# Kernel optimization log

Measured on AMD Instinct MI355X. Metric: run time of the kernel, lower is better.

Reference implementation:

```python
import jax, jax.numpy as jnp
import numpy as np

N, E, K, IN, OUT = 20000, 320000, 5, 256, 128
NAN_FRAC = 0.3


def setup_inputs() -> dict:
    key = jax.random.key(0)
    ks = jax.random.split(key, 8)
    x = jax.random.normal(ks[0], (N, IN), dtype=jnp.float32)
    nan_mask = jax.random.uniform(ks[1], (N, IN)) < NAN_FRAC
    x = jnp.where(nan_mask, jnp.nan, x)  # missing features as NaN
    edge_index = jax.random.randint(ks[2], (2, E), 0, N, dtype=jnp.int64)
    logp = jax.nn.log_softmax(jax.random.normal(ks[3], (K,), dtype=jnp.float32))
    means = jax.random.normal(ks[4], (K, IN), dtype=jnp.float32)
    logvars = jax.random.normal(ks[5], (K, IN), dtype=jnp.float32) * 0.1
    xav = 1.414 * np.sqrt(6.0 / (IN + OUT))
    weight = jax.random.uniform(ks[6], (IN, OUT), dtype=jnp.float32, minval=-xav, maxval=xav)
    bias = jnp.zeros((OUT,), dtype=jnp.float32)
    return {"x": x, "edge_index": edge_index, "logp": logp, "means": means,
            "logvars": logvars, "weight": weight, "bias": bias}


def _ex_relu(mu, sigma):
    # E[relu(X)] for X ~ N(mu, sigma); sigma is the variance
    sigma_s = jnp.where(sigma == 0, 1e-10, sigma)
    ss = jnp.sqrt(sigma_s)
    w = mu / ss
    nr = ss * (jnp.exp(-0.5 * w * w) / np.sqrt(2 * np.pi)
               + 0.5 * w * (1.0 + jax.lax.erf(w / np.sqrt(2))))
    return jnp.where(sigma == 0, jnp.maximum(mu, 0.0), nr)


def _gcn_norm(edge_index, num_nodes):
    # add self-loops, symmetric D^-1/2 A D^-1/2 normalization
    row = jnp.concatenate([edge_index[0], jnp.arange(num_nodes, dtype=edge_index.dtype)])
    col = jnp.concatenate([edge_index[1], jnp.arange(num_nodes, dtype=edge_index.dtype)])
    ones = jnp.ones(row.shape[0], dtype=jnp.float32)
    deg = jax.ops.segment_sum(ones, row, num_segments=num_nodes)
    dinv = jnp.where(deg > 0, jax.lax.rsqrt(deg), 0.0)
    wn = dinv[row] * dinv[col]
    return row, col, wn


def reference(x, edge_index, logp, means, logvars, weight, bias):
    n = x.shape[0]
    dim = x.shape[1]
    row, col, wn = _gcn_norm(edge_index, n)
    wn2 = wn * wn  # adj2 = adj * adj (elementwise on sparse values)

    isnan = jnp.isnan(x)                                       # [N, IN]
    variances = jnp.exp(logvars)                               # [K, IN]
    mean_mat = jnp.where(isnan[None], means[:, None, :], x[None])      # [K, N, IN]
    var_mat = jnp.where(isnan[None], variances[:, None, :], 0.0)       # [K, N, IN]

    transform_x = jnp.einsum('kni,io->kno', mean_mat, weight) + bias   # [K, N, OUT]
    transform_covs = jnp.einsum('kni,io->kno', var_mat, weight * weight)

    def spmm(vals, X):  # segment-sum SpMM: out[r] += vals_e * X[c]
        return jax.ops.segment_sum(X[col] * vals[:, None], row, num_segments=n)

    conv_x = jax.vmap(lambda X: spmm(wn, X))(transform_x)      # [K, N, OUT]
    conv_covs = jax.vmap(lambda X: spmm(wn2, X))(transform_covs)

    expected_x = _ex_relu(conv_x, conv_covs)                   # [K, N, OUT]

    # GMM responsibilities per node
    log_n = (-0.5 * jnp.sum((mean_mat - means[:, None, :]) ** 2 / variances[:, None, :], axis=2)
             - 0.5 * dim * np.log(2 * np.pi) - 0.5 * jnp.sum(logvars))  # [K, N]
    gamma = jax.nn.softmax(logp[:, None] + log_n, axis=0)      # [K, N]

    return jnp.sum(expected_x * gamma[:, :, None], axis=0)     # [N, OUT]
```

## Files before the change

### kernel.cpp

```cpp
#include <hip/hip_runtime.h>
#include <stdint.h>

#define N_NODES 20000
#define N_EDGES 320000
#define K_MIX 5
#define IN_F 256
#define OUT_F 128
#define NT 11
#define TC (NT * OUT_F)

typedef __attribute__((ext_vector_type(8))) short short8;
typedef __attribute__((ext_vector_type(4))) float floatx4;

__device__ __forceinline__ float bf2f(unsigned int u) {
  union { unsigned int i; float f; } v;
  v.i = (u & 0xffffu) << 16;
  return v.f;
}
__device__ __forceinline__ unsigned short f2bf(float f) {
  union { float f; unsigned int i; } v;
  v.f = f;
  unsigned int x = v.i;
  unsigned int r = (x + 0x7fffu + ((x >> 16) & 1u)) >> 16;
  return (unsigned short)r;
}

__device__ __forceinline__ float exrelu(float mu, float sig) {
  if (sig < 1e-30f) return fmaxf(mu, 0.f);
  float ss = sqrtf(sig);
  float w = mu / ss;
  float e = __expf(-0.5f * w * w);
  float axv = fabsf(w) * 0.70710678118654752f;
  float t = 1.f / (1.f + 0.3275911f * axv);
  float poly = t * (0.254829592f +
              t * (-0.284496736f +
              t * (1.421413741f +
              t * (-1.453152027f + t * 1.061405429f))));
  float erfv = 1.f - poly * e;
  erfv = copysignf(erfv, w);
  return ss * (e * 0.3989422804014327f + 0.5f * w * (1.f + erfv));
}

__global__ void k_deg(const int* __restrict__ row, int* __restrict__ deg) {
  int t = blockIdx.x * 256 + threadIdx.x;
  if (t < N_EDGES) atomicAdd(&deg[row[t]], 1);
}

__global__ void k_scan1(const int* __restrict__ deg, int* __restrict__ startofs,
                        int* __restrict__ bsums, float* __restrict__ dinv) {
  __shared__ int sd[256];
  int t = threadIdx.x;
  int i = blockIdx.x * 256 + t;
  int v = (i < N_NODES) ? deg[i] : 0;
  if (i < N_NODES) dinv[i] = rsqrtf((float)(v + 1));
  sd[t] = v;
  __syncthreads();
  for (int off = 1; off < 256; off <<= 1) {
    int u = (t >= off) ? sd[t - off] : 0;
    __syncthreads();
    sd[t] += u;
    __syncthreads();
  }
  if (i < N_NODES) startofs[i] = sd[t] - v;
  if (t == 255) bsums[blockIdx.x] = sd[255];
}

__global__ void k_scan2(int* __restrict__ bsums, int nb) {
  __shared__ int sd[128];
  int t = threadIdx.x;
  int v = (t < nb) ? bsums[t] : 0;
  sd[t] = v;
  __syncthreads();
  for (int off = 1; off < 128; off <<= 1) {
    int u = (t >= off) ? sd[t - off] : 0;
    __syncthreads();
    sd[t] += u;
    __syncthreads();
  }
  if (t < nb) bsums[t] = sd[t] - v;
}

__global__ void k_scan3(int* __restrict__ startofs, int* __restrict__ cursor,
                        const int* __restrict__ bsums) {
  int i = blockIdx.x * 256 + threadIdx.x;
  if (i < N_NODES) {
    int s0 = startofs[i] + bsums[blockIdx.x];
    startofs[i] = s0;
    cursor[i] = s0;
  }
}

__global__ void k_scatter(const int* __restrict__ row, const int* __restrict__ col,
                          const float* __restrict__ dinv, int* __restrict__ cursor,
                          int* __restrict__ csr_col, float* __restrict__ csr_w) {
  int t = blockIdx.x * 256 + threadIdx.x;
  if (t < N_EDGES) {
    int r = row[t], c = col[t];
    int p = atomicAdd(&cursor[r], 1);
    csr_col[p] = c;
    csr_w[p] = dinv[r] * dinv[c];
  }
}

__global__ void k_buildB(const float* __restrict__ W, const float* __restrict__ means,
                         const float* __restrict__ logvars, unsigned short* __restrict__ Bt) {
  int idx = blockIdx.x * 256 + threadIdx.x;
  int j = idx >> 15;
  int rem = idx & 32767;
  int n = rem >> 8;
  int kk = rem & 255;
  float wv = W[kk * OUT_F + n];
  float val;
  if (j == 0) val = wv;
  else if (j <= 5) val = means[(j - 1) * IN_F + kk] * wv;
  else val = expf(logvars[(j - 6) * IN_F + kk]) * wv * wv;
  Bt[idx] = f2bf(val);
}

__global__ void k_prepx(const float* __restrict__ x, const float* __restrict__ logp,
                        const float* __restrict__ means, const float* __restrict__ logvars,
                        unsigned short* __restrict__ X0, float* __restrict__ gamma) {
  __shared__ float s_mean[K_MIX * IN_F];
  __shared__ float s_rv[K_MIX * IN_F];
  int t = threadIdx.x;
  for (int j = t; j < K_MIX * IN_F; j += 256) {
    s_mean[j] = means[j];
    s_rv[j] = expf(-logvars[j]);
  }
  __syncthreads();
  int node = blockIdx.x * 4 + (t >> 6);
  if (node >= N_NODES) return;
  int lane = t & 63;
  float4 xv = *(const float4*)(x + (size_t)node * IN_F + 4 * lane);
  float xf[4] = {xv.x, xv.y, xv.z, xv.w};
  float gsum[K_MIX] = {0, 0, 0, 0, 0};
  ushort4 o;
  unsigned short* op = (unsigned short*)&o;
#pragma unroll
  for (int j = 0; j < 4; j++) {
    bool nn = (xf[j] != xf[j]);
    op[j] = nn ? (unsigned short)0x7FC0 : f2bf(xf[j]);
    if (!nn) {
      int fi = 4 * lane + j;
#pragma unroll
      for (int k = 0; k < K_MIX; k++) {
        float d = xf[j] - s_mean[k * IN_F + fi];
        gsum[k] += d * d * s_rv[k * IN_F + fi];
      }
    }
  }
  *(ushort4*)(X0 + node * IN_F + 4 * lane) = o;
#pragma unroll
  for (int k = 0; k < K_MIX; k++)
    for (int off = 32; off; off >>= 1) gsum[k] += __shfl_xor(gsum[k], off, 64);
  if (lane == 0) {
    float lg[K_MIX], mx = -1e30f;
#pragma unroll
    for (int k = 0; k < K_MIX; k++) {
      lg[k] = logp[k] - 0.5f * gsum[k];
      mx = fmaxf(mx, lg[k]);
    }
    float se = 0.f;
#pragma unroll
    for (int k = 0; k < K_MIX; k++) { lg[k] = expf(lg[k] - mx); se += lg[k]; }
    float inv = 1.f / se;
#pragma unroll
    for (int k = 0; k < K_MIX; k++) gamma[node * K_MIX + k] = lg[k] * inv;
  }
}

__global__ __launch_bounds__(64) void k_spmm(const unsigned short* __restrict__ X0,
                       const int* __restrict__ startofs, const int* __restrict__ deg,
                       const float* __restrict__ dinv, const int* __restrict__ csr_col,
                       const float* __restrict__ csr_w, unsigned short* __restrict__ G,
                       float* __restrict__ sArr) {
  int node = blockIdx.x;
  int lane = threadIdx.x;
  int fo = 4 * lane;
  float ax[4] = {0, 0, 0, 0}, am[4] = {0, 0, 0, 0}, am2[4] = {0, 0, 0, 0};
  float ssum = 0.f;
  float ws = dinv[node];
  ws = ws * ws;
  int st = startofs[node];
  int total = deg[node] + 1;
  ushort4 zero4 = {0, 0, 0, 0};
  ushort4 B0 = zero4, B1 = zero4, B2 = zero4, B3 = zero4,
          B4 = zero4, B5 = zero4, B6 = zero4, B7 = zero4;
  float W0 = 0.f, W1 = 0.f, W2 = 0.f, W3 = 0.f,
        W4 = 0.f, W5 = 0.f, W6 = 0.f, W7 = 0.f;
  B0 = *(const ushort4*)(X0 + node * IN_F + fo); W0 = ws;
#define PFILL(S)                                                      \
  if (S < total) {                                                    \
    int c = csr_col[st + (S - 1)];                                    \
    W##S = csr_w[st + (S - 1)];                                       \
    B##S = *(const ushort4*)(X0 + c * IN_F + fo);                     \
  }
  PFILL(1) PFILL(2) PFILL(3) PFILL(4) PFILL(5) PFILL(6) PFILL(7)
#undef PFILL

#define STEP(S)                                                       \
  if (W##S != 0.f) {                                                  \
    float wv = W##S, wv2 = wv * wv;                                   \
    ssum += wv;                                                       \
    const unsigned short* xp = (const unsigned short*)&B##S;          \
    _Pragma("unroll")                                                 \
    for (int j = 0; j < 4; j++) {                                     \
      float xf = bf2f(xp[j]);                                         \
      bool nn = (xf != xf);                                           \
      ax[j] = fmaf(wv, nn ? 0.f : xf, ax[j]);                         \
      am[j] += nn ? wv : 0.f;                                         \
      am2[j] += nn ? wv2 : 0.f;                                       \
    }                                                                 \
  }                                                                   \
  if (base + 8 + S < total) {                                         \
    int c = csr_col[st + base + 7 + S];                               \
    W##S = csr_w[st + base + 7 + S];                                  \
    B##S = *(const ushort4*)(X0 + c * IN_F + fo);                     \
  } else {                                                            \
    W##S = 0.f;                                                       \
  }

  for (int base = 0; base < total; base += 8) {
    STEP(0) STEP(1) STEP(2) STEP(3) STEP(4) STEP(5) STEP(6) STEP(7)
  }
#undef STEP

  ushort4 o;
  o.x = f2bf(ax[0]); o.y = f2bf(ax[1]); o.z = f2bf(ax[2]); o.w = f2bf(ax[3]);
  *(ushort4*)(G + node * 768 + fo) = o;
  o.x = f2bf(am[0]); o.y = f2bf(am[1]); o.z = f2bf(am[2]); o.w = f2bf(am[3]);
  *(ushort4*)(G + node * 768 + 256 + fo) = o;
  o.x = f2bf(am2[0]); o.y = f2bf(am2[1]); o.z = f2bf(am2[2]); o.w = f2bf(am2[3]);
  *(ushort4*)(G + node * 768 + 512 + fo) = o;
  if (lane == 0) sArr[node] = ssum;
}

__global__ __launch_bounds__(256) void k_gemm(const unsigned short* __restrict__ G,
                                              const unsigned short* __restrict__ Bt,
                                              unsigned short* __restrict__ T) {
  __shared__ char Als[128 * 64 * 2];
  __shared__ char Bls[128 * 64 * 2];
  int mt = blockIdx.x, jt = blockIdx.y;
  int aoff = (jt == 0) ? 0 : (jt <= 5 ? 256 : 512);
  int t = threadIdx.x, wave = t >> 6, lane = t & 63;
  int wr = wave >> 1, wc = wave & 1;
  int quad = lane >> 4, l16 = lane & 15;
  const unsigned short* Bp = Bt + (size_t)jt * 32768;

  floatx4 acc[4][4];
  floatx4 z = {0.f, 0.f, 0.f, 0.f};
#pragma unroll
  for (int mi = 0; mi < 4; mi++)
#pragma unroll
    for (int ni = 0; ni < 4; ni++) acc[mi][ni] = z;

  for (int k0 = 0; k0 < 256; k0 += 64) {
    __syncthreads();
#pragma unroll
    for (int i = 0; i < 4; i++) {
      int f = i * 256 + t;
      int r = f >> 3, cchunk = f & 7;
      int sw = cchunk ^ (r & 7);
      int gr = mt * 128 + r;
      if (gr >= N_NODES) gr = N_NODES - 1;
      *(uint4*)(Als + r * 128 + sw * 16) =
          *(const uint4*)(G + (size_t)gr * 768 + aoff + k0 + cchunk * 8);
      *(uint4*)(Bls + r * 128 + sw * 16) =
          *(const uint4*)(Bp + (size_t)r * 256 + k0 + cchunk * 8);
    }
    __syncthreads();
#pragma unroll
    for (int ks = 0; ks < 2; ks++) {
      int cc = ks * 4 + quad;
      short8 a[4], b[4];
#pragma unroll
      for (int mi = 0; mi < 4; mi++) {
        int r = wr * 64 + mi * 16 + l16;
        a[mi] = *(const short8*)(Als + r * 128 + (cc ^ (r & 7)) * 16);
      }
#pragma unroll
      for (int ni = 0; ni < 4; ni++) {
        int r = wc * 64 + ni * 16 + l16;
        b[ni] = *(const short8*)(Bls + r * 128 + (cc ^ (r & 7)) * 16);
      }
#pragma unroll
      for (int mi = 0; mi < 4; mi++)
#pragma unroll
        for (int ni = 0; ni < 4; ni++)
          acc[mi][ni] = __builtin_amdgcn_mfma_f32_16x16x32_bf16(a[mi], b[ni], acc[mi][ni], 0, 0, 0);
    }
  }
#pragma unroll
  for (int mi = 0; mi < 4; mi++)
#pragma unroll
    for (int ni = 0; ni < 4; ni++) {
      int gc = jt * 128 + wc * 64 + ni * 16 + l16;
#pragma unroll
      for (int reg = 0; reg < 4; reg++) {
        int gr = mt * 128 + wr * 64 + mi * 16 + quad * 4 + reg;
        if (gr < N_NODES) T[(size_t)gr * TC + gc] = f2bf(acc[mi][ni][reg]);
      }
    }
}

__global__ void k_final(const unsigned short* __restrict__ T, const float* __restrict__ gamma,
                        const float* __restrict__ sArr, const float* __restrict__ bias,
                        float* __restrict__ out) {
  int t = threadIdx.x;
  int node = blockIdx.x * 4 + (t >> 6);
  if (node >= N_NODES) return;
  int lane = t & 63;
  int o0 = 2 * lane;
  float g[K_MIX];
#pragma unroll
  for (int k = 0; k < K_MIX; k++) g[k] = gamma[node * K_MIX + k];
  float sv = sArr[node];
  float b0 = bias[o0], b1 = bias[o0 + 1];
  const unsigned short* Tr = T + (size_t)node * TC;
  unsigned int c0u = *(const unsigned int*)(Tr + o0);
  float cx0 = bf2f(c0u), cx1 = bf2f(c0u >> 16);
  float a0 = 0.f, a1 = 0.f;
#pragma unroll
  for (int k = 0; k < K_MIX; k++) {
    unsigned int tm = *(const unsigned int*)(Tr + 128 * (1 + k) + o0);
    unsigned int tv = *(const unsigned int*)(Tr + 128 * (6 + k) + o0);
    float mu0 = cx0 + bf2f(tm) + b0 * sv;
    float mu1 = cx1 + bf2f(tm >> 16) + b1 * sv;
    a0 += g[k] * exrelu(mu0, bf2f(tv));
    a1 += g[k] * exrelu(mu1, bf2f(tv >> 16));
  }
  float2 ov = {a0, a1};
  *(float2*)(out + (size_t)node * OUT_F + o0) = ov;
}

extern "C" void kernel_launch(void* const* d_in, const int* in_sizes, int n_in,
                              void* d_out, int out_size, void* d_ws, size_t ws_size,
                              hipStream_t stream) {
  const float* x = (const float*)d_in[0];
  const int* ei = (const int*)d_in[1];
  const float* logp = (const float*)d_in[2];
  const float* means = (const float*)d_in[3];
  const float* lvar = (const float*)d_in[4];
  const float* W = (const float*)d_in[5];
  const float* bias = (const float*)d_in[6];
  float* out = (float*)d_out;
  const int* row = ei;
  const int* col = ei + N_EDGES;

  char* p = (char*)d_ws;
  auto alloc = [&](size_t bytes) -> char* {
    char* q = p;
    p += (bytes + 255) & ~((size_t)255);
    return q;
  };
  int* deg = (int*)alloc(N_NODES * 4);
  float* dinv = (float*)alloc(N_NODES * 4);
  int* startofs = (int*)alloc(N_NODES * 4);
  int* cursor = (int*)alloc(N_NODES * 4);
  int* bsums = (int*)alloc(128 * 4);
  int* csr_col = (int*)alloc((size_t)N_EDGES * 4);
  float* csr_w = (float*)alloc((size_t)N_EDGES * 4);
  float* gamma = (float*)alloc((size_t)N_NODES * K_MIX * 4);
  float* sArr = (float*)alloc(N_NODES * 4);
  unsigned short* Bt = (unsigned short*)alloc((size_t)NT * 128 * 256 * 2);
  unsigned short* X0 = (unsigned short*)alloc((size_t)N_NODES * IN_F * 2);
  unsigned short* G = (unsigned short*)alloc((size_t)N_NODES * 768 * 2);
  unsigned short* T = (unsigned short*)alloc((size_t)N_NODES * TC * 2);

  hipMemsetAsync(deg, 0, N_NODES * 4, stream);
  k_deg<<<(N_EDGES + 255) / 256, 256, 0, stream>>>(row, deg);
  k_scan1<<<79, 256, 0, stream>>>(deg, startofs, bsums, dinv);
  k_scan2<<<1, 128, 0, stream>>>(bsums, 79);
  k_scan3<<<79, 256, 0, stream>>>(startofs, cursor, bsums);
  k_scatter<<<(N_EDGES + 255) / 256, 256, 0, stream>>>(row, col, dinv, cursor, csr_col, csr_w);
  k_buildB<<<(NT * 128 * 256) / 256, 256, 0, stream>>>(W, means, lvar, Bt);
  k_prepx<<<N_NODES / 4, 256, 0, stream>>>(x, logp, means, lvar, X0, gamma);
  k_spmm<<<N_NODES, 64, 0, stream>>>(X0, startofs, deg, dinv, csr_col, csr_w, G, sArr);
  k_gemm<<<dim3((N_NODES + 127) / 128, NT), 256, 0, stream>>>(G, Bt, T);
  k_final<<<N_NODES / 4, 256, 0, stream>>>(T, gamma, sArr, bias, out);
}
```

Before: 230.1 us.

## Fuse GEMM with expected-ReLU mixture epilogue, removing intermediate T buffer

```diff
diff --git a/kernel.cpp b/kernel.cpp
--- a/kernel.cpp
+++ b/kernel.cpp
@@ -7,7 +7,6 @@
 #define IN_F 256
 #define OUT_F 128
 #define NT 11
-#define TC (NT * OUT_F)
 
 typedef __attribute__((ext_vector_type(8))) short short8;
 typedef __attribute__((ext_vector_type(4))) float floatx4;
@@ -235,102 +234,87 @@
   if (lane == 0) sArr[node] = ssum;
 }
 
-__global__ __launch_bounds__(256) void k_gemm(const unsigned short* __restrict__ G,
-                                              const unsigned short* __restrict__ Bt,
-                                              unsigned short* __restrict__ T) {
-  __shared__ char Als[128 * 64 * 2];
-  __shared__ char Bls[128 * 64 * 2];
-  int mt = blockIdx.x, jt = blockIdx.y;
-  int aoff = (jt == 0) ? 0 : (jt <= 5 ? 256 : 512);
+__global__ __launch_bounds__(256) void k_gemmE(const unsigned short* __restrict__ G,
+                                               const unsigned short* __restrict__ Bt,
+                                               const float* __restrict__ gamma,
+                                               const float* __restrict__ sArr,
+                                               const float* __restrict__ bias,
+                                               float* __restrict__ out) {
+  __shared__ char Als[3 * 4 * 128 * 16];
+  __shared__ float lgam[128 * K_MIX];
+  __shared__ float ls[128];
+  int mt = blockIdx.x, ng = blockIdx.y;
+  int row0 = mt * 128;
   int t = threadIdx.x, wave = t >> 6, lane = t & 63;
-  int wr = wave >> 1, wc = wave & 1;
   int quad = lane >> 4, l16 = lane & 15;
-  const unsigned short* Bp = Bt + (size_t)jt * 32768;
-
-  floatx4 acc[4][4];
+
+  for (int i = t; i < 128 * K_MIX; i += 256) {
+    int node = row0 + i / K_MIX;
+    lgam[i] = (node < N_NODES) ? gamma[node * K_MIX + i % K_MIX] : 0.f;
+  }
+  if (t < 128) {
+    int node = row0 + t;
+    ls[t] = (node < N_NODES) ? sArr[node] : 0.f;
+  }
+  int colg = ng * 16 + l16;
+  float bc = bias[colg];
+  const unsigned short* Bcol = Bt + colg * 256 + quad * 8;
+
+  floatx4 acc[2][NT];
   floatx4 z = {0.f, 0.f, 0.f, 0.f};
 #pragma unroll
-  for (int mi = 0; mi < 4; mi++)
-#pragma unroll
-    for (int ni = 0; ni < 4; ni++) acc[mi][ni] = z;
-
-  for (int k0 = 0; k0 < 256; k0 += 64) {
-    __syncthreads();
-#pragma unroll
-    for (int i = 0; i < 4; i++) {
+  for (int m = 0; m < 2; m++)
+#pragma unroll
+    for (int j = 0; j < NT; j++) acc[m][j] = z;
+
+  int rbase = wave * 32;
+  for (int k0 = 0; k0 < 256; k0 += 32) {
+    __syncthreads();
+#pragma unroll
+    for (int i = 0; i < 6; i++) {
       int f = i * 256 + t;
-      int r = f >> 3, cchunk = f & 7;
-      int sw = cchunk ^ (r & 7);
-      int gr = mt * 128 + r;
+      int q = f & 3;
+      int r = (f >> 2) & 127;
+      int s = f >> 9;
+      int gr = row0 + r;
       if (gr >= N_NODES) gr = N_NODES - 1;
-      *(uint4*)(Als + r * 128 + sw * 16) =
-          *(const uint4*)(G + (size_t)gr * 768 + aoff + k0 + cchunk * 8);
-      *(uint4*)(Bls + r * 128 + sw * 16) =
-          *(const uint4*)(Bp + (size_t)r * 256 + k0 + cchunk * 8);
-    }
-    __syncthreads();
-#pragma unroll
-    for (int ks = 0; ks < 2; ks++) {
-      int cc = ks * 4 + quad;
-      short8 a[4], b[4];
-#pragma unroll
-      for (int mi = 0; mi < 4; mi++) {
-        int r = wr * 64 + mi * 16 + l16;
-        a[mi] = *(const short8*)(Als + r * 128 + (cc ^ (r & 7)) * 16);
+      *(uint4*)(Als + s * 8192 + q * 2048 + ((r ^ (q * 2)) & 127) * 16) =
+          *(const uint4*)(G + gr * 768 + s * 256 + k0 + q * 8);
+    }
+    __syncthreads();
+    short8 af[3][2];
+#pragma unroll
+    for (int s = 0; s < 3; s++)
+#pragma unroll
+      for (int m = 0; m < 2; m++) {
+        int r = rbase + m * 16 + l16;
+        af[s][m] = *(const short8*)(Als + s * 8192 + quad * 2048 +
+                                    ((r ^ (quad * 2)) & 127) * 16);
       }
 #pragma unroll
-      for (int ni = 0; ni < 4; ni++) {
-        int r = wc * 64 + ni * 16 + l16;
-        b[ni] = *(const short8*)(Bls + r * 128 + (cc ^ (r & 7)) * 16);
-      }
-#pragma unroll
-      for (int mi = 0; mi < 4; mi++)
-#pragma unroll
-        for (int ni = 0; ni < 4; ni++)
-          acc[mi][ni] = __builtin_amdgcn_mfma_f32_16x16x32_bf16(a[mi], b[ni], acc[mi][ni], 0, 0, 0);
-    }
-  }
-#pragma unroll
-  for (int mi = 0; mi < 4; mi++)
-#pragma unroll
-    for (int ni = 0; ni < 4; ni++) {
-      int gc = jt * 128 + wc * 64 + ni * 16 + l16;
-#pragma unroll
-      for (int reg = 0; reg < 4; reg++) {
-        int gr = mt * 128 + wr * 64 + mi * 16 + quad * 4 + reg;
-        if (gr < N_NODES) T[(size_t)gr * TC + gc] = f2bf(acc[mi][ni][reg]);
-      }
-    }
-}
-
-__global__ void k_final(const unsigned short* __restrict__ T, const float* __restrict__ gamma,
-                        const float* __restrict__ sArr, const float* __restrict__ bias,
-                        float* __restrict__ out) {
-  int t = threadIdx.x;
-  int node = blockIdx.x * 4 + (t >> 6);
-  if (node >= N_NODES) return;
-  int lane = t & 63;
-  int o0 = 2 * lane;
-  float g[K_MIX];
-#pragma unroll
-  for (int k = 0; k < K_MIX; k++) g[k] = gamma[node * K_MIX + k];
-  float sv = sArr[node];
-  float b0 = bias[o0], b1 = bias[o0 + 1];
-  const unsigned short* Tr = T + (size_t)node * TC;
-  unsigned int c0u = *(const unsigned int*)(Tr + o0);
-  float cx0 = bf2f(c0u), cx1 = bf2f(c0u >> 16);
-  float a0 = 0.f, a1 = 0.f;
-#pragma unroll
-  for (int k = 0; k < K_MIX; k++) {
-    unsigned int tm = *(const unsigned int*)(Tr + 128 * (1 + k) + o0);
-    unsigned int tv = *(const unsigned int*)(Tr + 128 * (6 + k) + o0);
-    float mu0 = cx0 + bf2f(tm) + b0 * sv;
-    float mu1 = cx1 + bf2f(tm >> 16) + b1 * sv;
-    a0 += g[k] * exrelu(mu0, bf2f(tv));
-    a1 += g[k] * exrelu(mu1, bf2f(tv >> 16));
-  }
-  float2 ov = {a0, a1};
-  *(float2*)(out + (size_t)node * OUT_F + o0) = ov;
+    for (int j = 0; j < NT; j++) {
+      int s = (j == 0) ? 0 : (j <= 5 ? 1 : 2);
+      short8 b = *(const short8*)(Bcol + j * 32768 + k0);
+      acc[0][j] = __builtin_amdgcn_mfma_f32_16x16x32_bf16(af[s][0], b, acc[0][j], 0, 0, 0);
+      acc[1][j] = __builtin_amdgcn_mfma_f32_16x16x32_bf16(af[s][1], b, acc[1][j], 0, 0, 0);
+    }
+  }
+
+#pragma unroll
+  for (int m = 0; m < 2; m++) {
+#pragma unroll
+    for (int reg = 0; reg < 4; reg++) {
+      int rl = rbase + m * 16 + quad * 4 + reg;
+      int node = row0 + rl;
+      float sv = ls[rl];
+      float cx = acc[m][0][reg] + bc * sv;
+      float a = 0.f;
+#pragma unroll
+      for (int k = 0; k < K_MIX; k++)
+        a += lgam[rl * K_MIX + k] * exrelu(cx + acc[m][1 + k][reg], acc[m][6 + k][reg]);
+      if (node < N_NODES) out[node * OUT_F + colg] = a;
+    }
+  }
 }
 
 extern "C" void kernel_launch(void* const* d_in, const int* in_sizes, int n_in,
@@ -365,7 +349,6 @@
   unsigned short* Bt = (unsigned short*)alloc((size_t)NT * 128 * 256 * 2);
   unsigned short* X0 = (unsigned short*)alloc((size_t)N_NODES * IN_F * 2);
   unsigned short* G = (unsigned short*)alloc((size_t)N_NODES * 768 * 2);
-  unsigned short* T = (unsigned short*)alloc((size_t)N_NODES * TC * 2);
 
   hipMemsetAsync(deg, 0, N_NODES * 4, stream);
   k_deg<<<(N_EDGES + 255) / 256, 256, 0, stream>>>(row, deg);
@@ -376,6 +359,5 @@
   k_buildB<<<(NT * 128 * 256) / 256, 256, 0, stream>>>(W, means, lvar, Bt);
   k_prepx<<<N_NODES / 4, 256, 0, stream>>>(x, logp, means, lvar, X0, gamma);
   k_spmm<<<N_NODES, 64, 0, stream>>>(X0, startofs, deg, dinv, csr_col, csr_w, G, sArr);
-  k_gemm<<<dim3((N_NODES + 127) / 128, NT), 256, 0, stream>>>(G, Bt, T);
-  k_final<<<N_NODES / 4, 256, 0, stream>>>(T, gamma, sArr, bias, out);
-}
+  k_gemmE<<<dim3((N_NODES + 127) / 128, 8), 256, 0, stream>>>(G, Bt, gamma, sArr, bias, out);
+}
```

New measurement: 283.7 us. +23.3%, slower.

## Precompute NaN mask in prep layout, hoist exp(-logvar), XCD-aware GEMM tile mapping

Applied to the files above, without the earlier changes.

```diff
diff --git a/kernel.cpp b/kernel.cpp
--- a/kernel.cpp
+++ b/kernel.cpp
@@ -8,6 +8,7 @@
 #define OUT_F 128
 #define NT 11
 #define TC (NT * OUT_F)
+#define BT_ELEMS (NT * 128 * 256)
 
 typedef __attribute__((ext_vector_type(8))) short short8;
 typedef __attribute__((ext_vector_type(4))) float floatx4;
@@ -15,6 +16,11 @@
 __device__ __forceinline__ float bf2f(unsigned int u) {
   union { unsigned int i; float f; } v;
   v.i = (u & 0xffffu) << 16;
+  return v.f;
+}
+__device__ __forceinline__ float bf2f_hi(unsigned int u) {
+  union { unsigned int i; float f; } v;
+  v.i = u & 0xffff0000u;
   return v.f;
 }
 __device__ __forceinline__ unsigned short f2bf(float f) {
@@ -103,53 +109,64 @@
 }
 
 __global__ void k_buildB(const float* __restrict__ W, const float* __restrict__ means,
-                         const float* __restrict__ logvars, unsigned short* __restrict__ Bt) {
+                         const float* __restrict__ logvars, unsigned short* __restrict__ Bt,
+                         float* __restrict__ rv) {
   int idx = blockIdx.x * 256 + threadIdx.x;
-  int j = idx >> 15;
-  int rem = idx & 32767;
-  int n = rem >> 8;
-  int kk = rem & 255;
-  float wv = W[kk * OUT_F + n];
-  float val;
-  if (j == 0) val = wv;
-  else if (j <= 5) val = means[(j - 1) * IN_F + kk] * wv;
-  else val = expf(logvars[(j - 6) * IN_F + kk]) * wv * wv;
-  Bt[idx] = f2bf(val);
+  if (idx < BT_ELEMS) {
+    int j = idx >> 15;
+    int rem = idx & 32767;
+    int n = rem >> 8;
+    int kk = rem & 255;
+    float wv = W[kk * OUT_F + n];
+    float val;
+    if (j == 0) val = wv;
+    else if (j <= 5) val = means[(j - 1) * IN_F + kk] * wv;
+    else val = expf(logvars[(j - 6) * IN_F + kk]) * wv * wv;
+    Bt[idx] = f2bf(val);
+  } else {
+    int r = idx - BT_ELEMS;
+    if (r < K_MIX * IN_F) rv[r] = expf(-logvars[r]);
+  }
 }
 
 __global__ void k_prepx(const float* __restrict__ x, const float* __restrict__ logp,
-                        const float* __restrict__ means, const float* __restrict__ logvars,
-                        unsigned short* __restrict__ X0, float* __restrict__ gamma) {
-  __shared__ float s_mean[K_MIX * IN_F];
-  __shared__ float s_rv[K_MIX * IN_F];
+                        const float* __restrict__ means, const float* __restrict__ rv,
+                        unsigned int* __restrict__ XP, float* __restrict__ gamma) {
   int t = threadIdx.x;
-  for (int j = t; j < K_MIX * IN_F; j += 256) {
-    s_mean[j] = means[j];
-    s_rv[j] = expf(-logvars[j]);
-  }
-  __syncthreads();
   int node = blockIdx.x * 4 + (t >> 6);
   if (node >= N_NODES) return;
   int lane = t & 63;
-  float4 xv = *(const float4*)(x + (size_t)node * IN_F + 4 * lane);
+  int fi = 4 * lane;
+  float4 xv = *(const float4*)(x + (size_t)node * IN_F + fi);
   float xf[4] = {xv.x, xv.y, xv.z, xv.w};
   float gsum[K_MIX] = {0, 0, 0, 0, 0};
-  ushort4 o;
-  unsigned short* op = (unsigned short*)&o;
+  unsigned short x0p[4], mp[4];
 #pragma unroll
   for (int j = 0; j < 4; j++) {
     bool nn = (xf[j] != xf[j]);
-    op[j] = nn ? (unsigned short)0x7FC0 : f2bf(xf[j]);
-    if (!nn) {
-      int fi = 4 * lane + j;
-#pragma unroll
-      for (int k = 0; k < K_MIX; k++) {
-        float d = xf[j] - s_mean[k * IN_F + fi];
-        gsum[k] += d * d * s_rv[k * IN_F + fi];
+    x0p[j] = nn ? (unsigned short)0 : f2bf(xf[j]);
+    mp[j] = nn ? (unsigned short)0x3F80 : (unsigned short)0;
+  }
+#pragma unroll
+  for (int k = 0; k < K_MIX; k++) {
+    float4 mk = *(const float4*)(means + k * IN_F + fi);
+    float4 rk = *(const float4*)(rv + k * IN_F + fi);
+    float mka[4] = {mk.x, mk.y, mk.z, mk.w};
+    float rka[4] = {rk.x, rk.y, rk.z, rk.w};
+#pragma unroll
+    for (int j = 0; j < 4; j++) {
+      if (xf[j] == xf[j]) {
+        float d = xf[j] - mka[j];
+        gsum[k] += d * d * rka[j];
       }
     }
   }
-  *(ushort4*)(X0 + node * IN_F + 4 * lane) = o;
+  uint4 o;
+  o.x = (unsigned int)x0p[0] | ((unsigned int)x0p[1] << 16);
+  o.y = (unsigned int)x0p[2] | ((unsigned int)x0p[3] << 16);
+  o.z = (unsigned int)mp[0] | ((unsigned int)mp[1] << 16);
+  o.w = (unsigned int)mp[2] | ((unsigned int)mp[3] << 16);
+  *(uint4*)(XP + node * 256 + 4 * lane) = o;
 #pragma unroll
   for (int k = 0; k < K_MIX; k++)
     for (int off = 32; off; off >>= 1) gsum[k] += __shfl_xor(gsum[k], off, 64);
@@ -162,14 +179,14 @@
     }
     float se = 0.f;
 #pragma unroll
-    for (int k = 0; k < K_MIX; k++) { lg[k] = expf(lg[k] - mx); se += lg[k]; }
+    for (int k = 0; k < K_MIX; k++) { lg[k] = __expf(lg[k] - mx); se += lg[k]; }
     float inv = 1.f / se;
 #pragma unroll
     for (int k = 0; k < K_MIX; k++) gamma[node * K_MIX + k] = lg[k] * inv;
   }
 }
 
-__global__ __launch_bounds__(64) void k_spmm(const unsigned short* __restrict__ X0,
+__global__ __launch_bounds__(64) void k_spmm(const unsigned int* __restrict__ XP,
                        const int* __restrict__ startofs, const int* __restrict__ deg,
                        const float* __restrict__ dinv, const int* __restrict__ csr_col,
                        const float* __restrict__ csr_w, unsigned short* __restrict__ G,
@@ -183,17 +200,17 @@
   ws = ws * ws;
   int st = startofs[node];
   int total = deg[node] + 1;
-  ushort4 zero4 = {0, 0, 0, 0};
-  ushort4 B0 = zero4, B1 = zero4, B2 = zero4, B3 = zero4,
-          B4 = zero4, B5 = zero4, B6 = zero4, B7 = zero4;
+  uint4 zero4 = {0, 0, 0, 0};
+  uint4 B0 = zero4, B1 = zero4, B2 = zero4, B3 = zero4,
+        B4 = zero4, B5 = zero4, B6 = zero4, B7 = zero4;
   float W0 = 0.f, W1 = 0.f, W2 = 0.f, W3 = 0.f,
         W4 = 0.f, W5 = 0.f, W6 = 0.f, W7 = 0.f;
-  B0 = *(const ushort4*)(X0 + node * IN_F + fo); W0 = ws;
+  B0 = *(const uint4*)(XP + node * 256 + fo); W0 = ws;
 #define PFILL(S)                                                      \
   if (S < total) {                                                    \
     int c = csr_col[st + (S - 1)];                                    \
     W##S = csr_w[st + (S - 1)];                                       \
-    B##S = *(const ushort4*)(X0 + c * IN_F + fo);                     \
+    B##S = *(const uint4*)(XP + c * 256 + fo);                        \
   }
   PFILL(1) PFILL(2) PFILL(3) PFILL(4) PFILL(5) PFILL(6) PFILL(7)
 #undef PFILL
@@ -202,20 +219,25 @@
   if (W##S != 0.f) {                                                  \
     float wv = W##S, wv2 = wv * wv;                                   \
     ssum += wv;                                                       \
-    const unsigned short* xp = (const unsigned short*)&B##S;          \
-    _Pragma("unroll")                                                 \
-    for (int j = 0; j < 4; j++) {                                     \
-      float xf = bf2f(xp[j]);                                         \
-      bool nn = (xf != xf);                                           \
-      ax[j] = fmaf(wv, nn ? 0.f : xf, ax[j]);                         \
-      am[j] += nn ? wv : 0.f;                                         \
-      am2[j] += nn ? wv2 : 0.f;                                       \
-    }                                                                 \
+    ax[0] = fmaf(wv, bf2f(B##S.x), ax[0]);                            \
+    ax[1] = fmaf(wv, bf2f_hi(B##S.x), ax[1]);                         \
+    ax[2] = fmaf(wv, bf2f(B##S.y), ax[2]);                            \
+    ax[3] = fmaf(wv, bf2f_hi(B##S.y), ax[3]);                         \
+    float m0 = bf2f(B##S.z), m1 = bf2f_hi(B##S.z);                    \
+    float m2 = bf2f(B##S.w), m3 = bf2f_hi(B##S.w);                    \
+    am[0] = fmaf(wv, m0, am[0]);                                      \
+    am[1] = fmaf(wv, m1, am[1]);                                      \
+    am[2] = fmaf(wv, m2, am[2]);                                      \
+    am[3] = fmaf(wv, m3, am[3]);                                      \
+    am2[0] = fmaf(wv2, m0, am2[0]);                                   \
+    am2[1] = fmaf(wv2, m1, am2[1]);                                   \
+    am2[2] = fmaf(wv2, m2, am2[2]);                                   \
+    am2[3] = fmaf(wv2, m3, am2[3]);                                   \
   }                                                                   \
   if (base + 8 + S < total) {                                         \
     int c = csr_col[st + base + 7 + S];                               \
     W##S = csr_w[st + base + 7 + S];                                  \
-    B##S = *(const ushort4*)(X0 + c * IN_F + fo);                     \
+    B##S = *(const uint4*)(XP + c * 256 + fo);                        \
   } else {                                                            \
     W##S = 0.f;                                                       \
   }
@@ -240,7 +262,12 @@
                                               unsigned short* __restrict__ T) {
   __shared__ char Als[128 * 64 * 2];
   __shared__ char Bls[128 * 64 * 2];
-  int mt = blockIdx.x, jt = blockIdx.y;
+  int id = blockIdx.x;
+  int xcd = id & 7;
+  int s2 = id >> 3;
+  int jt = s2 % 11;
+  int mt = xcd + 8 * (s2 / 11);
+  if (mt * 128 >= N_NODES) return;
   int aoff = (jt == 0) ? 0 : (jt <= 5 ? 256 : 512);
   int t = threadIdx.x, wave = t >> 6, lane = t & 63;
   int wr = wave >> 1, wc = wave & 1;
@@ -318,16 +345,16 @@
   float b0 = bias[o0], b1 = bias[o0 + 1];
   const unsigned short* Tr = T + (size_t)node * TC;
   unsigned int c0u = *(const unsigned int*)(Tr + o0);
-  float cx0 = bf2f(c0u), cx1 = bf2f(c0u >> 16);
+  float cx0 = bf2f(c0u), cx1 = bf2f_hi(c0u);
   float a0 = 0.f, a1 = 0.f;
 #pragma unroll
   for (int k = 0; k < K_MIX; k++) {
     unsigned int tm = *(const unsigned int*)(Tr + 128 * (1 + k) + o0);
     unsigned int tv = *(const unsigned int*)(Tr + 128 * (6 + k) + o0);
     float mu0 = cx0 + bf2f(tm) + b0 * sv;
-    float mu1 = cx1 + bf2f(tm >> 16) + b1 * sv;
+    float mu1 = cx1 + bf2f_hi(tm) + b1 * sv;
     a0 += g[k] * exrelu(mu0, bf2f(tv));
-    a1 += g[k] * exrelu(mu1, bf2f(tv >> 16));
+    a1 += g[k] * exrelu(mu1, bf2f_hi(tv));
   }
   float2 ov = {a0, a1};
   *(float2*)(out + (size_t)node * OUT_F + o0) = ov;
@@ -362,8 +389,9 @@
   float* csr_w = (float*)alloc((size_t)N_EDGES * 4);
   float* gamma = (float*)alloc((size_t)N_NODES * K_MIX * 4);
   float* sArr = (float*)alloc(N_NODES * 4);
-  unsigned short* Bt = (unsigned short*)alloc((size_t)NT * 128 * 256 * 2);
-  unsigned short* X0 = (unsigned short*)alloc((size_t)N_NODES * IN_F * 2);
+  float* rv = (float*)alloc(K_MIX * IN_F * 4);
+  unsigned short* Bt = (unsigned short*)alloc((size_t)BT_ELEMS * 2);
+  unsigned int* XP = (unsigned int*)alloc((size_t)N_NODES * 256 * 4);
   unsigned short* G = (unsigned short*)alloc((size_t)N_NODES * 768 * 2);
   unsigned short* T = (unsigned short*)alloc((size_t)N_NODES * TC * 2);
 
@@ -373,9 +401,9 @@
   k_scan2<<<1, 128, 0, stream>>>(bsums, 79);
   k_scan3<<<79, 256, 0, stream>>>(startofs, cursor, bsums);
   k_scatter<<<(N_EDGES + 255) / 256, 256, 0, stream>>>(row, col, dinv, cursor, csr_col, csr_w);
-  k_buildB<<<(NT * 128 * 256) / 256, 256, 0, stream>>>(W, means, lvar, Bt);
-  k_prepx<<<N_NODES / 4, 256, 0, stream>>>(x, logp, means, lvar, X0, gamma);
-  k_spmm<<<N_NODES, 64, 0, stream>>>(X0, startofs, deg, dinv, csr_col, csr_w, G, sArr);
-  k_gemm<<<dim3((N_NODES + 127) / 128, NT), 256, 0, stream>>>(G, Bt, T);
+  k_buildB<<<(BT_ELEMS + K_MIX * IN_F + 255) / 256, 256, 0, stream>>>(W, means, lvar, Bt, rv);
+  k_prepx<<<N_NODES / 4, 256, 0, stream>>>(x, logp, means, rv, XP, gamma);
+  k_spmm<<<N_NODES, 64, 0, stream>>>(XP, startofs, deg, dinv, csr_col, csr_w, G, sArr);
+  k_gemm<<<8 * 20 * 11, 256, 0, stream>>>(G, Bt, T);
   k_final<<<N_NODES / 4, 256, 0, stream>>>(T, gamma, sArr, bias, out);
 }
```

New measurement: 239.5 us. 1.04x slower.
